# Kernel optimization log

Hardware: AMD Instinct MI355X
Metric: run time of the kernel (lower is better)

The kernel has to match this reference:

```python
import jax, jax.numpy as jnp
import numpy as np

B = 4096
FEATURES = 4608 + 4608 + 8 + 1  # 9225
LSTM = 512
R = FEATURES / LSTM
D1 = int(FEATURES / R ** (1.0 / 3.0))
D2 = int(FEATURES / R ** (2.0 / 3.0))
ACTION_SHAPES = (64, 64, 64, 64, 64, 64, 64, 64)


def setup_inputs() -> dict:
    key = jax.random.key(0)
    ks = jax.random.split(key, 32)
    s = 0.02
    inp = {
        "actualCanvasFeatures": jax.random.normal(ks[0], (B, 4608), jnp.float32),
        "objectiveCanvasFeatures": jax.random.normal(ks[1], (B, 4608), jnp.float32),
        "last_action": jax.random.uniform(ks[2], (B, 8), jnp.float32),
        "episode_percentage": 0,
        # encoder MLP
        "W1": jax.random.normal(ks[3], (FEATURES, D1), jnp.float32) * s,
        "b1": jnp.zeros((D1,), jnp.float32),
        "W2": jax.random.normal(ks[4], (D1, D2), jnp.float32) * s,
        "b2": jnp.zeros((D2,), jnp.float32),
        "W3": jax.random.normal(ks[5], (D2, LSTM), jnp.float32) * s,
        "b3": jnp.zeros((LSTM,), jnp.float32),
        # LSTM (torch gate order i,f,g,o)
        "Wih": jax.random.normal(ks[6], (4 * LSTM, LSTM), jnp.float32) * s,
        "Whh": jax.random.normal(ks[7], (4 * LSTM, LSTM), jnp.float32) * s,
        "bih": jnp.zeros((4 * LSTM,), jnp.float32),
        "bhh": jnp.zeros((4 * LSTM,), jnp.float32),
        "h0": jnp.zeros((B, LSTM), jnp.float32),
        "c0": jnp.zeros((B, LSTM), jnp.float32),
        # decoder
        "dW1": jax.random.normal(ks[8], (LSTM, LSTM // 2), jnp.float32) * s,
        "db1": jnp.zeros((LSTM // 2,), jnp.float32),
        "headWs": tuple(jax.random.normal(ks[9 + i], (LSTM // 2, a), jnp.float32) * s
                        for i, a in enumerate(ACTION_SHAPES)),
        "headbs": tuple(jnp.zeros((a,), jnp.float32) for a in ACTION_SHAPES),
        "dWo": jax.random.normal(ks[20], (LSTM + 1, LSTM), jnp.float32) * s,
        "dbo": jnp.zeros((LSTM,), jnp.float32),
    }
    return inp


def reference(actualCanvasFeatures, objectiveCanvasFeatures, last_action,
              episode_percentage, W1, b1, W2, b2, W3, b3, Wih, Whh, bih, bhh,
              h0, c0, dW1, db1, headWs, headbs, dWo, dbo):
    b = actualCanvasFeatures.shape[0]
    ep = jnp.full((b, 1), episode_percentage, dtype=jnp.float32)
    feats = jnp.concatenate(
        [actualCanvasFeatures, objectiveCanvasFeatures, last_action, ep], axis=1)
    # encoder MLP (dropout is eval-mode identity)
    x = jax.nn.relu(feats @ W1 + b1)
    x = jax.nn.relu(x @ W2 + b2)
    x = jax.nn.relu(x @ W3 + b3)
    # single-step LSTM cell, torch gate order i,f,g,o
    gates = x @ Wih.T + bih + h0 @ Whh.T + bhh
    i, f, g, o = jnp.split(gates, 4, axis=1)
    c = jax.nn.sigmoid(f) * c0 + jax.nn.sigmoid(i) * jnp.tanh(g)
    z = jax.nn.sigmoid(o) * jnp.tanh(c)  # seed
    key = jax.random.key(42)
    actions = []
    log_probabilities = jnp.zeros((b,), jnp.float32)
    entropy = jnp.float32(0.0)
    for Wk, bk in zip(headWs, headbs):
        z1 = jax.nn.relu(z @ dW1 + db1)
        logits = z1 @ Wk + bk
        logp = jax.nn.log_softmax(logits, axis=1)
        probs = jnp.exp(logp)
        key, sk = jax.random.split(key)
        act = jax.random.categorical(sk, logits, axis=1)  # [b] int
        actions.append(act.astype(jnp.float32))
        entropy = entropy + jnp.sum(-jnp.sum(probs * logp, axis=1))
        log_probabilities = log_probabilities + jnp.take_along_axis(
            logp, act[:, None], axis=1)[:, 0]
        z = jax.nn.relu(
            jnp.concatenate([z, act.astype(jnp.float32)[:, None]], axis=1) @ dWo + dbo)
    action = jnp.stack(actions, axis=1)  # [b, n_sub_actions]
    return action, entropy, log_probabilities
```

## Files before the change

kernel.cpp:

```cpp
#include <hip/hip_runtime.h>
#include <cstdint>
#include <cstring>

typedef _Float16 f16;
typedef _Float16 f16x8 __attribute__((ext_vector_type(8)));
typedef float f32x4 __attribute__((ext_vector_type(4)));

static constexpr int kPartitionable = 1;

struct Ptr8 { const float* p[8]; };
struct Keys8 { uint32_t k[8][2]; };

__device__ __host__ __forceinline__ int swz(int r, int k) {
  return k ^ ((r & 7) << 3);
}

__device__ __forceinline__ void gload16(const void* g, void* l) {
  __builtin_amdgcn_global_load_lds(
      (const __attribute__((address_space(1))) unsigned int*)g,
      (__attribute__((address_space(3))) unsigned int*)l, 16, 0, 0);
}

__host__ __device__ inline void tf2x32(uint32_t k0, uint32_t k1,
                                       uint32_t x0, uint32_t x1,
                                       uint32_t& o0, uint32_t& o1) {
  uint32_t ks[3] = {k0, k1, k0 ^ k1 ^ 0x1BD11BDAu};
  uint32_t v0 = x0 + ks[0], v1 = x1 + ks[1];
  const int r0[4] = {13, 15, 26, 6};
  const int r1[4] = {17, 29, 16, 24};
  for (int g = 0; g < 5; ++g) {
    const int* rr = (g & 1) ? r1 : r0;
    for (int j = 0; j < 4; ++j) {
      v0 += v1;
      v1 = (v1 << rr[j]) | (v1 >> (32 - rr[j]));
      v1 ^= v0;
    }
    v0 += ks[(g + 1) % 3];
    v1 += ks[(g + 2) % 3] + (uint32_t)(g + 1);
  }
  o0 = v0; o1 = v1;
}

template <int BM, int BN>
__global__ __launch_bounds__(256, 2) void gemm_split(
    const f16* __restrict__ Ah, const f16* __restrict__ Al, int lda,
    const f16* __restrict__ Bh, const f16* __restrict__ Bl, int ldb,
    int K,
    const float* __restrict__ bias1, const float* __restrict__ bias2,
    int nReal, int relu, int writeF32,
    float* __restrict__ outF, f16* __restrict__ outH, f16* __restrict__ outL,
    int ldo) {
  constexpr int BK = 64;
  constexpr int TM = BM / 32;
  constexpr int TN = BN / 32;
  static_assert(BM == BN, "square tiles only");
  __shared__ f16 sAh[BM * BK];
  __shared__ f16 sAl[BM * BK];
  __shared__ f16 sBh[BN * BK];
  __shared__ f16 sBl[BN * BK];

  const int tid = threadIdx.x;
  const int wave = tid >> 6;
  const int lane = tid & 63;
  const int wm = wave & 1, wn = wave >> 1;
  const int m0 = blockIdx.x * BM;
  const int n0 = blockIdx.y * BN;

  f32x4 acc[TM][TN];
  const f32x4 zero = {0.f, 0.f, 0.f, 0.f};
#pragma unroll
  for (int i = 0; i < TM; ++i)
#pragma unroll
    for (int j = 0; j < TN; ++j) acc[i][j] = zero;

  const f16* src;
  f16* dst;
  int ld, base;
  if (wave == 0)      { src = Ah; dst = sAh; ld = lda; base = m0; }
  else if (wave == 1) { src = Al; dst = sAl; ld = lda; base = m0; }
  else if (wave == 2) { src = Bh; dst = sBh; ld = ldb; base = n0; }
  else                { src = Bl; dst = sBl; ld = ldb; base = n0; }
  constexpr int NITER = BM / 8;
  const f16* gbase = src + (size_t)(base + (lane >> 3)) * ld + (lane & 7) * 8;

  const int fr = lane & 15;
  const int q8 = (lane >> 4) * 8;
  const int sw = (fr & 7) << 3;

  for (int k0 = 0; k0 < K; k0 += BK) {
    __syncthreads();
#pragma unroll
    for (int j = 0; j < NITER; ++j)
      gload16(gbase + (size_t)(j * 8) * ld + k0, dst + j * 512);
    __syncthreads();
#pragma unroll
    for (int kk = 0; kk < BK; kk += 32) {
      const int kf = (kk + q8) ^ sw;
      f16x8 aH[TM], aL[TM], bH[TN], bL[TN];
#pragma unroll
      for (int i = 0; i < TM; ++i) {
        int off = (wm * (BM / 2) + i * 16 + fr) * BK + kf;
        aH[i] = *(const f16x8*)&sAh[off];
        aL[i] = *(const f16x8*)&sAl[off];
      }
#pragma unroll
      for (int j = 0; j < TN; ++j) {
        int off = (wn * (BN / 2) + j * 16 + fr) * BK + kf;
        bH[j] = *(const f16x8*)&sBh[off];
        bL[j] = *(const f16x8*)&sBl[off];
      }
#pragma unroll
      for (int i = 0; i < TM; ++i)
#pragma unroll
        for (int j = 0; j < TN; ++j) {
          acc[i][j] = __builtin_amdgcn_mfma_f32_16x16x32_f16(aH[i], bH[j], acc[i][j], 0, 0, 0);
          acc[i][j] = __builtin_amdgcn_mfma_f32_16x16x32_f16(aH[i], bL[j], acc[i][j], 0, 0, 0);
          acc[i][j] = __builtin_amdgcn_mfma_f32_16x16x32_f16(aL[i], bH[j], acc[i][j], 0, 0, 0);
        }
    }
  }
  const int rq = lane >> 4, cl = lane & 15;
#pragma unroll
  for (int i = 0; i < TM; ++i)
#pragma unroll
    for (int j = 0; j < TN; ++j)
#pragma unroll
      for (int r = 0; r < 4; ++r) {
        int row = m0 + wm * (BM / 2) + i * 16 + rq * 4 + r;
        int col = n0 + wn * (BN / 2) + j * 16 + cl;
        float v = acc[i][j][r];
        if (col < nReal) {
          if (bias1) v += bias1[col];
          if (bias2) v += bias2[col];
          if (relu) v = fmaxf(v, 0.f);
        } else {
          v = 0.f;
        }
        if (writeF32) {
          outF[(size_t)row * ldo + col] = v;
        } else {
          size_t o = (size_t)row * ldo + swz(row, col);
          f16 h = (f16)v;
          outH[o] = h;
          outL[o] = (f16)(v - (float)h);
        }
      }
}

__global__ void conv_feats(const float* __restrict__ A, const float* __restrict__ O,
                           const float* __restrict__ LA, const int* __restrict__ EP,
                           f16* __restrict__ H, f16* __restrict__ L) {
  uint32_t idx = blockIdx.x * 256u + threadIdx.x;
  if (idx >= 4096u * 1160u) return;
  uint32_t b = idx / 1160u;
  uint32_t c = (idx - b * 1160u) * 8u;
  float v[8];
  if (c < 4608u) {
    const float4* p = (const float4*)(A + (size_t)b * 4608 + c);
    float4 x = p[0], y = p[1];
    v[0] = x.x; v[1] = x.y; v[2] = x.z; v[3] = x.w;
    v[4] = y.x; v[5] = y.y; v[6] = y.z; v[7] = y.w;
  } else if (c < 9216u) {
    const float4* p = (const float4*)(O + (size_t)b * 4608 + (c - 4608u));
    float4 x = p[0], y = p[1];
    v[0] = x.x; v[1] = x.y; v[2] = x.z; v[3] = x.w;
    v[4] = y.x; v[5] = y.y; v[6] = y.z; v[7] = y.w;
  } else if (c == 9216u) {
#pragma unroll
    for (int j = 0; j < 8; ++j) v[j] = LA[(size_t)b * 8 + j];
  } else if (c == 9224u) {
    v[0] = (float)EP[0];
#pragma unroll
    for (int j = 1; j < 8; ++j) v[j] = 0.f;
  } else {
#pragma unroll
    for (int j = 0; j < 8; ++j) v[j] = 0.f;
  }
  size_t o = (size_t)b * 9280 + ((int)c ^ (((int)b & 7) << 3));
  f16x8 hv, lv;
#pragma unroll
  for (int j = 0; j < 8; ++j) {
    f16 h = (f16)v[j];
    hv[j] = h;
    lv[j] = (f16)(v[j] - (float)h);
  }
  *(f16x8*)&H[o] = hv;
  *(f16x8*)&L[o] = lv;
}

__global__ void convT_kernel(const float* __restrict__ W, int Kreal, int Nreal,
                             f16* __restrict__ BtH, f16* __restrict__ BtL, int Kpad) {
  __shared__ float tile[32][33];
  int k0 = blockIdx.x * 32, n0 = blockIdx.y * 32;
  int tx = threadIdx.x, ty = threadIdx.y;
  for (int r = 0; r < 32; r += 8) {
    int k = k0 + ty + r, n = n0 + tx;
    float v = (k < Kreal && n < Nreal) ? W[(size_t)k * Nreal + n] : 0.f;
    tile[ty + r][tx] = v;
  }
  __syncthreads();
  for (int r = 0; r < 32; r += 8) {
    int n = n0 + ty + r, k = k0 + tx;
    float v = tile[tx][ty + r];
    size_t o = (size_t)n * Kpad + swz(n, k);
    f16 h = (f16)v;
    BtH[o] = h;
    BtL[o] = (f16)(v - (float)h);
  }
}

__global__ void conv_fm(const float* __restrict__ W, int Kreal, int Nreal, int NT, int KC,
                        f16* __restrict__ FH, f16* __restrict__ FL) {
  int idx = blockIdx.x * 256 + threadIdx.x;
  if (idx >= NT * KC * 64) return;
  int lane = idx & 63;
  int t = idx >> 6;
  int kc = t % KC, ntile = t / KC;
  int n = ntile * 16 + (lane & 15);
  int k0 = kc * 32 + (lane >> 4) * 8;
  f16x8 hv, lv;
#pragma unroll
  for (int j = 0; j < 8; ++j) {
    int k = k0 + j;
    float v = (k < Kreal && n < Nreal) ? W[(size_t)k * Nreal + n] : 0.f;
    f16 h = (f16)v;
    hv[j] = h;
    lv[j] = (f16)(v - (float)h);
  }
  *(f16x8*)&FH[(size_t)idx * 8] = hv;
  *(f16x8*)&FL[(size_t)idx * 8] = lv;
}

__global__ void conv_fm_heads(Ptr8 ws, f16* __restrict__ FH, f16* __restrict__ FL) {
  int h = blockIdx.y;
  int idx = blockIdx.x * 256 + threadIdx.x;
  if (idx >= 2048) return;
  int lane = idx & 63;
  int t = idx >> 6;
  int kc = t & 7, ntile = t >> 3;
  int n = ntile * 16 + (lane & 15);
  int k0 = kc * 32 + (lane >> 4) * 8;
  const float* W = ws.p[h];
  f16x8 hv, lv;
#pragma unroll
  for (int j = 0; j < 8; ++j) {
    float v = W[(size_t)(k0 + j) * 64 + n];
    f16 hh = (f16)v;
    hv[j] = hh;
    lv[j] = (f16)(v - (float)hh);
  }
  size_t base = (size_t)h * 16384 + (size_t)idx * 8;
  *(f16x8*)&FH[base] = hv;
  *(f16x8*)&FL[base] = lv;
}

__global__ void conv_lstmB(const float* __restrict__ Wih, const float* __restrict__ Whh,
                           f16* __restrict__ H, f16* __restrict__ L) {
  uint32_t idx = blockIdx.x * 256u + threadIdx.x;
  uint32_t n = idx >> 10, k = idx & 1023u;
  float v = (k < 512u) ? Wih[(size_t)n * 512 + k] : Whh[(size_t)n * 512 + (k - 512u)];
  size_t o = (size_t)n * 1024 + swz((int)n, (int)k);
  f16 h = (f16)v;
  H[o] = h;
  L[o] = (f16)(v - (float)h);
}

__global__ void conv_h0(const float* __restrict__ h0, f16* __restrict__ H, f16* __restrict__ L) {
  uint32_t idx = blockIdx.x * 256u + threadIdx.x;
  uint32_t b = idx >> 9, j = idx & 511u;
  float v = h0[idx];
  size_t o = (size_t)b * 1024 + swz((int)b, (int)(512 + j));
  f16 h = (f16)v;
  H[o] = h;
  L[o] = (f16)(v - (float)h);
}

__global__ void lstm_pointwise(const float* __restrict__ gates, const float* __restrict__ c0,
                               f16* __restrict__ zH, f16* __restrict__ zL) {
  uint32_t idx = blockIdx.x * 256u + threadIdx.x;
  uint32_t b = idx >> 9, n = idx & 511u;
  const float* g = gates + (size_t)b * 2048;
  float gi = g[n], gf = g[512 + n], gg = g[1024 + n], go = g[1536 + n];
  float si = 1.f / (1.f + expf(-gi));
  float sf = 1.f / (1.f + expf(-gf));
  float so = 1.f / (1.f + expf(-go));
  float c = sf * c0[idx] + si * tanhf(gg);
  float z = so * tanhf(c);
  size_t o = (size_t)b * 576 + swz((int)b, (int)n);
  f16 h = (f16)z;
  zH[o] = h;
  zL[o] = (f16)(z - (float)h);
}

__global__ void init_pads(f16* __restrict__ zAH, f16* __restrict__ zAL,
                          float* __restrict__ out) {
  uint32_t idx = blockIdx.x * 256u + threadIdx.x;
  if (idx < 4096u * 8u) {
    uint32_t b = idx >> 3, c8 = 512u + (idx & 7u) * 8u;
    f16x8 zz = {0, 0, 0, 0, 0, 0, 0, 0};
    *(f16x8*)&zAH[(size_t)b * 576 + c8] = zz;
    *(f16x8*)&zAL[(size_t)b * 576 + c8] = zz;
  }
  if (idx == 0) out[32768] = 0.f;
}

__device__ inline double shfl_xor_dbl(double v, int m) {
  union { double d; int i[2]; } u;
  u.d = v;
  u.i[0] = __shfl_xor(u.i[0], m);
  u.i[1] = __shfl_xor(u.i[1], m);
  return u.d;
}

__global__ __launch_bounds__(256, 1) void decoder_fused(
    const f16* __restrict__ zH0, const f16* __restrict__ zL0,
    const f16* __restrict__ FM1h, const f16* __restrict__ FM1l,
    const float* __restrict__ db1,
    const f16* __restrict__ FMhh, const f16* __restrict__ FMhl,
    Ptr8 hb,
    const f16* __restrict__ FMoh, const f16* __restrict__ FMol,
    const float* __restrict__ dbo,
    Keys8 sk, int partitionable, float* __restrict__ out) {
  constexpr int ZS = 576, Z1S = 256;
  __shared__ f16 zbH[32 * ZS], zbL[32 * ZS];
  __shared__ f16 z1H[32 * Z1S], z1L[32 * Z1S];
  __shared__ float lgt[32 * 64];
  __shared__ float entSh[4];
  const int tid = threadIdx.x;
  const int wave = tid >> 6, lane = tid & 63;
  const int fr = lane & 15, rq = lane >> 4, q8 = rq * 8;
  const int sw = (fr & 7) << 3;
  const int b0 = blockIdx.x * 32;
  const f32x4 zero = {0.f, 0.f, 0.f, 0.f};

  for (int t = tid; t < 2304; t += 256) {
    ((f16x8*)zbH)[t] = ((const f16x8*)(zH0 + (size_t)b0 * ZS))[t];
    ((f16x8*)zbL)[t] = ((const f16x8*)(zL0 + (size_t)b0 * ZS))[t];
  }
  float entAcc = 0.f;
  float logpAcc[8] = {0.f, 0.f, 0.f, 0.f, 0.f, 0.f, 0.f, 0.f};

  for (int h = 0; h < 8; ++h) {
    __syncthreads();
    {
      f32x4 acc[2][4];
#pragma unroll
      for (int i = 0; i < 2; ++i)
#pragma unroll
        for (int j = 0; j < 4; ++j) acc[i][j] = zero;
      for (int kc = 0; kc < 16; ++kc) {
        int kf = (kc * 32 + q8) ^ sw;
        f16x8 aH[2], aL[2];
#pragma unroll
        for (int i = 0; i < 2; ++i) {
          int off = (i * 16 + fr) * ZS + kf;
          aH[i] = *(const f16x8*)&zbH[off];
          aL[i] = *(const f16x8*)&zbL[off];
        }
#pragma unroll
        for (int j = 0; j < 4; ++j) {
          size_t fo = (size_t)((wave * 4 + j) * 16 + kc) * 512 + lane * 8;
          f16x8 bH = *(const f16x8*)&FM1h[fo];
          f16x8 bL = *(const f16x8*)&FM1l[fo];
#pragma unroll
          for (int i = 0; i < 2; ++i) {
            acc[i][j] = __builtin_amdgcn_mfma_f32_16x16x32_f16(aH[i], bH, acc[i][j], 0, 0, 0);
            acc[i][j] = __builtin_amdgcn_mfma_f32_16x16x32_f16(aH[i], bL, acc[i][j], 0, 0, 0);
            acc[i][j] = __builtin_amdgcn_mfma_f32_16x16x32_f16(aL[i], bH, acc[i][j], 0, 0, 0);
          }
        }
      }
#pragma unroll
      for (int j = 0; j < 4; ++j) {
        int col = (wave * 4 + j) * 16 + fr;
        float bb = db1[col];
#pragma unroll
        for (int i = 0; i < 2; ++i)
#pragma unroll
          for (int r = 0; r < 4; ++r) {
            int row = i * 16 + rq * 4 + r;
            float v = fmaxf(acc[i][j][r] + bb, 0.f);
            f16 hv = (f16)v;
            int po = row * Z1S + (col ^ ((row & 7) << 3));
            z1H[po] = hv;
            z1L[po] = (f16)(v - (float)hv);
          }
      }
    }
    __syncthreads();
    {
      f32x4 acc2[2] = {zero, zero};
      const int r0 = (wave & 1) * 16;
      const int tb = (wave >> 1) * 2;
      for (int kc = 0; kc < 8; ++kc) {
        int kf = (kc * 32 + q8) ^ sw;
        int off = (r0 + fr) * Z1S + kf;
        f16x8 aH = *(const f16x8*)&z1H[off];
        f16x8 aL = *(const f16x8*)&z1L[off];
#pragma unroll
        for (int j = 0; j < 2; ++j) {
          size_t fo = (size_t)(h * 32 + (tb + j) * 8 + kc) * 512 + lane * 8;
          f16x8 bH = *(const f16x8*)&FMhh[fo];
          f16x8 bL = *(const f16x8*)&FMhl[fo];
          acc2[j] = __builtin_amdgcn_mfma_f32_16x16x32_f16(aH, bH, acc2[j], 0, 0, 0);
          acc2[j] = __builtin_amdgcn_mfma_f32_16x16x32_f16(aH, bL, acc2[j], 0, 0, 0);
          acc2[j] = __builtin_amdgcn_mfma_f32_16x16x32_f16(aL, bH, acc2[j], 0, 0, 0);
        }
      }
#pragma unroll
      for (int j = 0; j < 2; ++j) {
        int col = (tb + j) * 16 + fr;
        float bb = hb.p[h][col];
#pragma unroll
        for (int r = 0; r < 4; ++r) lgt[(r0 + rq * 4 + r) * 64 + col] = acc2[j][r] + bb;
      }
    }
    __syncthreads();
    for (int rr = 0; rr < 8; ++rr) {
      int row = wave * 8 + rr;
      int b = b0 + row;
      float l = lgt[row * 64 + lane];
      uint32_t i = (uint32_t)b * 64u + (uint32_t)lane;
      uint32_t bits;
      if (partitionable) {
        uint32_t o0, o1;
        tf2x32(sk.k[h][0], sk.k[h][1], 0u, i, o0, o1);
        bits = o0 ^ o1;
      } else {
        const uint32_t Hh = 131072u;
        uint32_t c0, c1, o0, o1;
        int pick;
        if (i < Hh) { c0 = i; c1 = i + Hh; pick = 0; }
        else        { c0 = i - Hh; c1 = i; pick = 1; }
        tf2x32(sk.k[h][0], sk.k[h][1], c0, c1, o0, o1);
        bits = pick ? o1 : o0;
      }
      uint32_t ub = (bits >> 9) | 0x3f800000u;
      float u;
      __builtin_memcpy(&u, &ub, 4);
      u -= 1.0f;
      if (u == 0.0f) u = 1.17549435e-38f;
      double gum = -log(-log((double)u));
      double s = (double)l + gum;
      int bi = lane;
      double bv = s;
#pragma unroll
      for (int off = 1; off < 64; off <<= 1) {
        double ov = shfl_xor_dbl(bv, off);
        int oi = __shfl_xor(bi, off);
        if (ov > bv || (ov == bv && oi < bi)) { bv = ov; bi = oi; }
      }
      int act = bi;
      float m = l;
#pragma unroll
      for (int off = 1; off < 64; off <<= 1) m = fmaxf(m, __shfl_xor(m, off));
      float e = expf(l - m);
      float S = e, D = e * l;
#pragma unroll
      for (int off = 1; off < 64; off <<= 1) {
        S += __shfl_xor(S, off);
        D += __shfl_xor(D, off);
      }
      float M = m + logf(S);
      entAcc += (M - D / S);
      float l_act = __shfl(l, act);
      logpAcc[rr] += (l_act - M);
      if (lane == 0) {
        out[(size_t)b * 8 + h] = (float)act;
        int po = row * ZS + (512 ^ ((row & 7) << 3));
        zbH[po] = (f16)act;
        zbL[po] = (f16)0.f;
      }
    }
    __syncthreads();
    {
      f32x4 acc4[2][8];
#pragma unroll
      for (int i = 0; i < 2; ++i)
#pragma unroll
        for (int j = 0; j < 8; ++j) acc4[i][j] = zero;
      for (int kc = 0; kc < 18; ++kc) {
        int kf = (kc * 32 + q8) ^ sw;
        f16x8 aH[2], aL[2];
#pragma unroll
        for (int i = 0; i < 2; ++i) {
          int off = (i * 16 + fr) * ZS + kf;
          aH[i] = *(const f16x8*)&zbH[off];
          aL[i] = *(const f16x8*)&zbL[off];
        }
#pragma unroll
        for (int j = 0; j < 8; ++j) {
          size_t fo = (size_t)((wave * 8 + j) * 18 + kc) * 512 + lane * 8;
          f16x8 bH = *(const f16x8*)&FMoh[fo];
          f16x8 bL = *(const f16x8*)&FMol[fo];
#pragma unroll
          for (int i = 0; i < 2; ++i) {
            acc4[i][j] = __builtin_amdgcn_mfma_f32_16x16x32_f16(aH[i], bH, acc4[i][j], 0, 0, 0);
            acc4[i][j] = __builtin_amdgcn_mfma_f32_16x16x32_f16(aH[i], bL, acc4[i][j], 0, 0, 0);
            acc4[i][j] = __builtin_amdgcn_mfma_f32_16x16x32_f16(aL[i], bH, acc4[i][j], 0, 0, 0);
          }
        }
      }
      __syncthreads();
#pragma unroll
      for (int j = 0; j < 8; ++j) {
        int col = wave * 128 + j * 16 + fr;
        float bb = dbo[col];
#pragma unroll
        for (int i = 0; i < 2; ++i)
#pragma unroll
          for (int r = 0; r < 4; ++r) {
            int row = i * 16 + rq * 4 + r;
            float v = fmaxf(acc4[i][j][r] + bb, 0.f);
            f16 hv = (f16)v;
            int po = row * ZS + (col ^ ((row & 7) << 3));
            zbH[po] = hv;
            zbL[po] = (f16)(v - (float)hv);
          }
      }
    }
  }
  if (lane == 0) entSh[wave] = entAcc;
  __syncthreads();
  if (tid == 0) atomicAdd(&out[32768], entSh[0] + entSh[1] + entSh[2] + entSh[3]);
  if (lane == 0) {
#pragma unroll
    for (int rr = 0; rr < 8; ++rr) out[32769 + b0 + wave * 8 + rr] = logpAcc[rr];
  }
}

extern "C" void kernel_launch(void* const* d_in, const int* in_sizes, int n_in,
                              void* d_out, int out_size, void* d_ws, size_t ws_size,
                              hipStream_t stream) {
  (void)in_sizes; (void)out_size; (void)ws_size;
  const float* actual = (const float*)d_in[0];
  const float* object = (const float*)d_in[1];
  const float* lastA = (const float*)d_in[2];
  const int* ep = (const int*)d_in[3];
  const float* W1 = (const float*)d_in[4];
  const float* b1 = (const float*)d_in[5];
  const float* W2 = (const float*)d_in[6];
  const float* b2 = (const float*)d_in[7];
  const float* W3 = (const float*)d_in[8];
  const float* b3 = (const float*)d_in[9];
  const float* Wih = (const float*)d_in[10];
  const float* Whh = (const float*)d_in[11];
  const float* bih = (const float*)d_in[12];
  const float* bhh = (const float*)d_in[13];
  const float* h0 = (const float*)d_in[14];
  const float* c0 = (const float*)d_in[15];
  const float* dW1 = (const float*)d_in[16];
  const float* db1 = (const float*)d_in[17];
  const float* headW[8];
  const float* headb[8];
  const float *dWo, *dbo;
  if (n_in >= 36) {
    for (int h = 0; h < 8; ++h) headW[h] = (const float*)d_in[18 + h];
    for (int h = 0; h < 8; ++h) headb[h] = (const float*)d_in[26 + h];
    dWo = (const float*)d_in[34];
    dbo = (const float*)d_in[35];
  } else {
    const float* hw = (const float*)d_in[18];
    const float* hbp = (const float*)d_in[19];
    for (int h = 0; h < 8; ++h) { headW[h] = hw + (size_t)h * 256 * 64; headb[h] = hbp + (size_t)h * 64; }
    dWo = (const float*)d_in[20];
    dbo = (const float*)d_in[21];
  }

  constexpr int Bq = 4096;
  constexpr int K1 = 9280, N1 = 3584, N1r = 3518;
  constexpr int K2 = 3584, N2 = 1408, N2r = 1342;
  constexpr int K3 = 1408, N3 = 512;
  constexpr int KL = 1024, NL = 2048;

  uint8_t* w = (uint8_t*)d_ws;
  size_t off = 0;
  auto alloc = [&](size_t bytes) -> void* {
    off = (off + 1023) & ~(size_t)1023;
    void* p = w + off;
    off += bytes;
    return p;
  };
  f16* A1h = (f16*)alloc((size_t)Bq * K1 * 2);
  f16* A1l = (f16*)alloc((size_t)Bq * K1 * 2);
  f16* Bt1h = (f16*)alloc((size_t)N1 * K1 * 2);
  f16* Bt1l = (f16*)alloc((size_t)N1 * K1 * 2);
  f16* x1h = (f16*)alloc((size_t)Bq * K2 * 2);
  f16* x1l = (f16*)alloc((size_t)Bq * K2 * 2);
  f16* Bt2h = (f16*)alloc((size_t)N2 * K2 * 2);
  f16* Bt2l = (f16*)alloc((size_t)N2 * K2 * 2);
  size_t poff = 0;
  auto palloc = [&](size_t bytes) -> void* {
    poff = (poff + 1023) & ~(size_t)1023;
    void* p = w + poff;
    poff += bytes;
    return p;
  };
  f16* x2h = (f16*)palloc((size_t)Bq * K3 * 2);
  f16* x2l = (f16*)palloc((size_t)Bq * K3 * 2);
  f16* Bt3h = (f16*)palloc((size_t)N3 * K3 * 2);
  f16* Bt3l = (f16*)palloc((size_t)N3 * K3 * 2);
  f16* ALh = (f16*)palloc((size_t)Bq * KL * 2);
  f16* ALl = (f16*)palloc((size_t)Bq * KL * 2);
  f16* BLh = (f16*)palloc((size_t)NL * KL * 2);
  f16* BLl = (f16*)palloc((size_t)NL * KL * 2);
  float* gates = (float*)palloc((size_t)Bq * NL * 4);
  f16* zAH = (f16*)palloc((size_t)Bq * 576 * 2);
  f16* zAL = (f16*)palloc((size_t)Bq * 576 * 2);
  f16* FM1h = (f16*)palloc((size_t)16 * 16 * 512 * 2);
  f16* FM1l = (f16*)palloc((size_t)16 * 16 * 512 * 2);
  f16* FMhh = (f16*)palloc((size_t)8 * 32 * 512 * 2);
  f16* FMhl = (f16*)palloc((size_t)8 * 32 * 512 * 2);
  f16* FMoh = (f16*)palloc((size_t)32 * 18 * 512 * 2);
  f16* FMol = (f16*)palloc((size_t)32 * 18 * 512 * 2);

  uint32_t k0 = 0u, k1 = 42u;
  Keys8 sk;
  for (int h = 0; h < 8; ++h) {
    if (kPartitionable) {
      uint32_t a0, a1, b0v, b1v;
      tf2x32(k0, k1, 0u, 0u, a0, a1);
      tf2x32(k0, k1, 0u, 1u, b0v, b1v);
      sk.k[h][0] = b0v; sk.k[h][1] = b1v;
      k0 = a0; k1 = a1;
    } else {
      uint32_t a0, a1, b0v, b1v;
      tf2x32(k0, k1, 0u, 2u, a0, a1);
      tf2x32(k0, k1, 1u, 3u, b0v, b1v);
      sk.k[h][0] = a1; sk.k[h][1] = b1v;
      k0 = a0; k1 = b0v;
    }
  }
  Ptr8 hws, hbs;
  for (int h = 0; h < 8; ++h) { hws.p[h] = headW[h]; hbs.p[h] = headb[h]; }

  dim3 blk(256);
  dim3 tblk(32, 8);

  conv_feats<<<(4096u * 1160u + 255) / 256, blk, 0, stream>>>(actual, object, lastA, ep, A1h, A1l);
  convT_kernel<<<dim3(K1 / 32, N1 / 32), tblk, 0, stream>>>(W1, 9225, 3518, Bt1h, Bt1l, K1);
  convT_kernel<<<dim3(K2 / 32, N2 / 32), tblk, 0, stream>>>(W2, 3518, 1342, Bt2h, Bt2l, K2);

  gemm_split<128, 128><<<dim3(Bq / 128, N1 / 128), blk, 0, stream>>>(
      A1h, A1l, K1, Bt1h, Bt1l, K1, K1, b1, nullptr, N1r, 1, 0, nullptr, x1h, x1l, K2);

  init_pads<<<(4096u * 8u + 255) / 256, blk, 0, stream>>>(zAH, zAL, (float*)d_out);
  convT_kernel<<<dim3(K3 / 32, N3 / 32), tblk, 0, stream>>>(W3, 1342, 512, Bt3h, Bt3l, K3);
  conv_lstmB<<<(2048u * 1024u) / 256, blk, 0, stream>>>(Wih, Whh, BLh, BLl);
  conv_h0<<<(4096u * 512u) / 256, blk, 0, stream>>>(h0, ALh, ALl);
  conv_fm<<<(16 * 16 * 64 + 255) / 256, blk, 0, stream>>>(dW1, 512, 256, 16, 16, FM1h, FM1l);
  conv_fm<<<(32 * 18 * 64 + 255) / 256, blk, 0, stream>>>(dWo, 513, 512, 32, 18, FMoh, FMol);
  conv_fm_heads<<<dim3(8, 8), blk, 0, stream>>>(hws, FMhh, FMhl);

  gemm_split<128, 128><<<dim3(Bq / 128, N2 / 128), blk, 0, stream>>>(
      x1h, x1l, K2, Bt2h, Bt2l, K2, K2, b2, nullptr, N2r, 1, 0, nullptr, x2h, x2l, K3);
  gemm_split<128, 128><<<dim3(Bq / 128, N3 / 128), blk, 0, stream>>>(
      x2h, x2l, K3, Bt3h, Bt3l, K3, K3, b3, nullptr, N3, 1, 0, nullptr, ALh, ALl, KL);
  gemm_split<128, 128><<<dim3(Bq / 128, NL / 128), blk, 0, stream>>>(
      ALh, ALl, KL, BLh, BLl, KL, KL, bih, bhh, NL, 0, 1, gates, nullptr, nullptr, NL);
  lstm_pointwise<<<(4096u * 512u) / 256, blk, 0, stream>>>(gates, c0, zAH, zAL);

  decoder_fused<<<128, blk, 0, stream>>>(
      zAH, zAL, FM1h, FM1l, db1, FMhh, FMhl, hbs, FMoh, FMol, dbo,
      sk, kPartitionable, (float*)d_out);
}
```

Before: 1.883 ms.

## Double-buffer split GEMM with 8 waves and halve decoder batch per block

The split-fp16 GEMM moves to 512-thread blocks with double-buffered LDS stages, so global-to-LDS loads for the next K tile are issued while the current tile is computed. This replaces the two-barrier load-then-compute loop. Each wave now holds a 64x32 sub-tile, and LDS use grows to 128KB per block, limiting occupancy to one block per CU. Separately, the fused decoder processes 16 rows per block instead of 32 and launches 256 blocks, spreading the serial decode across more CUs at the cost of less weight reuse per block.

```diff
diff --git a/kernel.cpp b/kernel.cpp
--- a/kernel.cpp
+++ b/kernel.cpp
@@ -41,8 +41,7 @@
   o0 = v0; o1 = v1;
 }
 
-template <int BM, int BN>
-__global__ __launch_bounds__(256, 2) void gemm_split(
+__global__ __launch_bounds__(512, 1) void gemm_split(
     const f16* __restrict__ Ah, const f16* __restrict__ Al, int lda,
     const f16* __restrict__ Bh, const f16* __restrict__ Bl, int ldb,
     int K,
@@ -50,84 +49,95 @@
     int nReal, int relu, int writeF32,
     float* __restrict__ outF, f16* __restrict__ outH, f16* __restrict__ outL,
     int ldo) {
-  constexpr int BK = 64;
-  constexpr int TM = BM / 32;
-  constexpr int TN = BN / 32;
-  static_assert(BM == BN, "square tiles only");
-  __shared__ f16 sAh[BM * BK];
-  __shared__ f16 sAl[BM * BK];
-  __shared__ f16 sBh[BN * BK];
-  __shared__ f16 sBl[BN * BK];
+  __shared__ f16 sAh0[8192], sAl0[8192], sBh0[8192], sBl0[8192];
+  __shared__ f16 sAh1[8192], sAl1[8192], sBh1[8192], sBl1[8192];
 
   const int tid = threadIdx.x;
   const int wave = tid >> 6;
   const int lane = tid & 63;
   const int wm = wave & 1, wn = wave >> 1;
-  const int m0 = blockIdx.x * BM;
-  const int n0 = blockIdx.y * BN;
-
-  f32x4 acc[TM][TN];
+  const int m0 = blockIdx.x * 128;
+  const int n0 = blockIdx.y * 128;
+
+  f32x4 acc[4][2];
   const f32x4 zero = {0.f, 0.f, 0.f, 0.f};
 #pragma unroll
-  for (int i = 0; i < TM; ++i)
-#pragma unroll
-    for (int j = 0; j < TN; ++j) acc[i][j] = zero;
-
+  for (int i = 0; i < 4; ++i)
+#pragma unroll
+    for (int j = 0; j < 2; ++j) acc[i][j] = zero;
+
+  const int arr = wave >> 1, p = wave & 1;
   const f16* src;
-  f16* dst;
+  f16 *l0, *l1;
   int ld, base;
-  if (wave == 0)      { src = Ah; dst = sAh; ld = lda; base = m0; }
-  else if (wave == 1) { src = Al; dst = sAl; ld = lda; base = m0; }
-  else if (wave == 2) { src = Bh; dst = sBh; ld = ldb; base = n0; }
-  else                { src = Bl; dst = sBl; ld = ldb; base = n0; }
-  constexpr int NITER = BM / 8;
-  const f16* gbase = src + (size_t)(base + (lane >> 3)) * ld + (lane & 7) * 8;
+  if (arr == 0)      { src = Ah; l0 = sAh0; l1 = sAh1; ld = lda; base = m0; }
+  else if (arr == 1) { src = Al; l0 = sAl0; l1 = sAl1; ld = lda; base = m0; }
+  else if (arr == 2) { src = Bh; l0 = sBh0; l1 = sBh1; ld = ldb; base = n0; }
+  else               { src = Bl; l0 = sBl0; l1 = sBl1; ld = ldb; base = n0; }
+  l0 += p * 4096;
+  l1 += p * 4096;
+  const f16* gbase = src + (size_t)(base + p * 64 + (lane >> 3)) * ld + (lane & 7) * 8;
 
   const int fr = lane & 15;
   const int q8 = (lane >> 4) * 8;
   const int sw = (fr & 7) << 3;
 
-  for (int k0 = 0; k0 < K; k0 += BK) {
-    __syncthreads();
-#pragma unroll
-    for (int j = 0; j < NITER; ++j)
-      gload16(gbase + (size_t)(j * 8) * ld + k0, dst + j * 512);
-    __syncthreads();
-#pragma unroll
-    for (int kk = 0; kk < BK; kk += 32) {
+  auto stage = [&](int k0, f16* lb) {
+#pragma unroll
+    for (int j = 0; j < 8; ++j)
+      gload16(gbase + (size_t)(j * 8) * ld + k0, lb + j * 512);
+  };
+  auto compute = [&](const f16* cAh, const f16* cAl, const f16* cBh, const f16* cBl) {
+#pragma unroll
+    for (int kk = 0; kk < 64; kk += 32) {
       const int kf = (kk + q8) ^ sw;
-      f16x8 aH[TM], aL[TM], bH[TN], bL[TN];
-#pragma unroll
-      for (int i = 0; i < TM; ++i) {
-        int off = (wm * (BM / 2) + i * 16 + fr) * BK + kf;
-        aH[i] = *(const f16x8*)&sAh[off];
-        aL[i] = *(const f16x8*)&sAl[off];
-      }
-#pragma unroll
-      for (int j = 0; j < TN; ++j) {
-        int off = (wn * (BN / 2) + j * 16 + fr) * BK + kf;
-        bH[j] = *(const f16x8*)&sBh[off];
-        bL[j] = *(const f16x8*)&sBl[off];
-      }
-#pragma unroll
-      for (int i = 0; i < TM; ++i)
-#pragma unroll
-        for (int j = 0; j < TN; ++j) {
+      f16x8 aH[4], aL[4], bH[2], bL[2];
+#pragma unroll
+      for (int i = 0; i < 4; ++i) {
+        int off = (wm * 64 + i * 16 + fr) * 64 + kf;
+        aH[i] = *(const f16x8*)&cAh[off];
+        aL[i] = *(const f16x8*)&cAl[off];
+      }
+#pragma unroll
+      for (int j = 0; j < 2; ++j) {
+        int off = (wn * 32 + j * 16 + fr) * 64 + kf;
+        bH[j] = *(const f16x8*)&cBh[off];
+        bL[j] = *(const f16x8*)&cBl[off];
+      }
+#pragma unroll
+      for (int i = 0; i < 4; ++i)
+#pragma unroll
+        for (int j = 0; j < 2; ++j) {
           acc[i][j] = __builtin_amdgcn_mfma_f32_16x16x32_f16(aH[i], bH[j], acc[i][j], 0, 0, 0);
           acc[i][j] = __builtin_amdgcn_mfma_f32_16x16x32_f16(aH[i], bL[j], acc[i][j], 0, 0, 0);
           acc[i][j] = __builtin_amdgcn_mfma_f32_16x16x32_f16(aL[i], bH[j], acc[i][j], 0, 0, 0);
         }
     }
-  }
+  };
+
+  const int nT = K >> 6;
+  stage(0, l0);
+  int t = 0;
+  while (true) {
+    __syncthreads();
+    if (t + 1 < nT) stage((t + 1) * 64, l1);
+    compute(sAh0, sAl0, sBh0, sBl0);
+    if (++t == nT) break;
+    __syncthreads();
+    if (t + 1 < nT) stage((t + 1) * 64, l0);
+    compute(sAh1, sAl1, sBh1, sBl1);
+    if (++t == nT) break;
+  }
+
   const int rq = lane >> 4, cl = lane & 15;
 #pragma unroll
-  for (int i = 0; i < TM; ++i)
-#pragma unroll
-    for (int j = 0; j < TN; ++j)
+  for (int i = 0; i < 4; ++i)
+#pragma unroll
+    for (int j = 0; j < 2; ++j)
 #pragma unroll
       for (int r = 0; r < 4; ++r) {
-        int row = m0 + wm * (BM / 2) + i * 16 + rq * 4 + r;
-        int col = n0 + wn * (BN / 2) + j * 16 + cl;
+        int row = m0 + wm * 64 + i * 16 + rq * 4 + r;
+        int col = n0 + wn * 32 + j * 16 + cl;
         float v = acc[i][j][r];
         if (col < nReal) {
           if (bias1) v += bias1[col];
@@ -322,52 +332,42 @@
     const float* __restrict__ dbo,
     Keys8 sk, int partitionable, float* __restrict__ out) {
   constexpr int ZS = 576, Z1S = 256;
-  __shared__ f16 zbH[32 * ZS], zbL[32 * ZS];
-  __shared__ f16 z1H[32 * Z1S], z1L[32 * Z1S];
-  __shared__ float lgt[32 * 64];
+  __shared__ f16 zbH[16 * ZS], zbL[16 * ZS];
+  __shared__ f16 z1H[16 * Z1S], z1L[16 * Z1S];
+  __shared__ float lgt[16 * 64];
   __shared__ float entSh[4];
   const int tid = threadIdx.x;
   const int wave = tid >> 6, lane = tid & 63;
   const int fr = lane & 15, rq = lane >> 4, q8 = rq * 8;
   const int sw = (fr & 7) << 3;
-  const int b0 = blockIdx.x * 32;
+  const int b0 = blockIdx.x * 16;
   const f32x4 zero = {0.f, 0.f, 0.f, 0.f};
 
-  for (int t = tid; t < 2304; t += 256) {
+  for (int t = tid; t < 1152; t += 256) {
     ((f16x8*)zbH)[t] = ((const f16x8*)(zH0 + (size_t)b0 * ZS))[t];
     ((f16x8*)zbL)[t] = ((const f16x8*)(zL0 + (size_t)b0 * ZS))[t];
   }
   float entAcc = 0.f;
-  float logpAcc[8] = {0.f, 0.f, 0.f, 0.f, 0.f, 0.f, 0.f, 0.f};
+  float logpAcc[4] = {0.f, 0.f, 0.f, 0.f};
 
   for (int h = 0; h < 8; ++h) {
     __syncthreads();
     {
-      f32x4 acc[2][4];
-#pragma unroll
-      for (int i = 0; i < 2; ++i)
-#pragma unroll
-        for (int j = 0; j < 4; ++j) acc[i][j] = zero;
+      f32x4 acc[4];
+#pragma unroll
+      for (int j = 0; j < 4; ++j) acc[j] = zero;
       for (int kc = 0; kc < 16; ++kc) {
         int kf = (kc * 32 + q8) ^ sw;
-        f16x8 aH[2], aL[2];
-#pragma unroll
-        for (int i = 0; i < 2; ++i) {
-          int off = (i * 16 + fr) * ZS + kf;
-          aH[i] = *(const f16x8*)&zbH[off];
-          aL[i] = *(const f16x8*)&zbL[off];
-        }
+        f16x8 aH = *(const f16x8*)&zbH[fr * ZS + kf];
+        f16x8 aL = *(const f16x8*)&zbL[fr * ZS + kf];
 #pragma unroll
         for (int j = 0; j < 4; ++j) {
           size_t fo = (size_t)((wave * 4 + j) * 16 + kc) * 512 + lane * 8;
           f16x8 bH = *(const f16x8*)&FM1h[fo];
           f16x8 bL = *(const f16x8*)&FM1l[fo];
-#pragma unroll
-          for (int i = 0; i < 2; ++i) {
-            acc[i][j] = __builtin_amdgcn_mfma_f32_16x16x32_f16(aH[i], bH, acc[i][j], 0, 0, 0);
-            acc[i][j] = __builtin_amdgcn_mfma_f32_16x16x32_f16(aH[i], bL, acc[i][j], 0, 0, 0);
-            acc[i][j] = __builtin_amdgcn_mfma_f32_16x16x32_f16(aL[i], bH, acc[i][j], 0, 0, 0);
-          }
+          acc[j] = __builtin_amdgcn_mfma_f32_16x16x32_f16(aH, bH, acc[j], 0, 0, 0);
+          acc[j] = __builtin_amdgcn_mfma_f32_16x16x32_f16(aH, bL, acc[j], 0, 0, 0);
+          acc[j] = __builtin_amdgcn_mfma_f32_16x16x32_f16(aL, bH, acc[j], 0, 0, 0);
         }
       }
 #pragma unroll
@@ -375,49 +375,38 @@
         int col = (wave * 4 + j) * 16 + fr;
         float bb = db1[col];
 #pragma unroll
-        for (int i = 0; i < 2; ++i)
-#pragma unroll
-          for (int r = 0; r < 4; ++r) {
-            int row = i * 16 + rq * 4 + r;
-            float v = fmaxf(acc[i][j][r] + bb, 0.f);
-            f16 hv = (f16)v;
-            int po = row * Z1S + (col ^ ((row & 7) << 3));
-            z1H[po] = hv;
-            z1L[po] = (f16)(v - (float)hv);
-          }
+        for (int r = 0; r < 4; ++r) {
+          int row = rq * 4 + r;
+          float v = fmaxf(acc[j][r] + bb, 0.f);
+          f16 hv = (f16)v;
+          int po = row * Z1S + (col ^ ((row & 7) << 3));
+          z1H[po] = hv;
+          z1L[po] = (f16)(v - (float)hv);
+        }
       }
     }
     __syncthreads();
     {
-      f32x4 acc2[2] = {zero, zero};
-      const int r0 = (wave & 1) * 16;
-      const int tb = (wave >> 1) * 2;
+      f32x4 acc2 = zero;
       for (int kc = 0; kc < 8; ++kc) {
         int kf = (kc * 32 + q8) ^ sw;
-        int off = (r0 + fr) * Z1S + kf;
-        f16x8 aH = *(const f16x8*)&z1H[off];
-        f16x8 aL = *(const f16x8*)&z1L[off];
-#pragma unroll
-        for (int j = 0; j < 2; ++j) {
-          size_t fo = (size_t)(h * 32 + (tb + j) * 8 + kc) * 512 + lane * 8;
-          f16x8 bH = *(const f16x8*)&FMhh[fo];
-          f16x8 bL = *(const f16x8*)&FMhl[fo];
-          acc2[j] = __builtin_amdgcn_mfma_f32_16x16x32_f16(aH, bH, acc2[j], 0, 0, 0);
-          acc2[j] = __builtin_amdgcn_mfma_f32_16x16x32_f16(aH, bL, acc2[j], 0, 0, 0);
-          acc2[j] = __builtin_amdgcn_mfma_f32_16x16x32_f16(aL, bH, acc2[j], 0, 0, 0);
-        }
-      }
-#pragma unroll
-      for (int j = 0; j < 2; ++j) {
-        int col = (tb + j) * 16 + fr;
-        float bb = hb.p[h][col];
-#pragma unroll
-        for (int r = 0; r < 4; ++r) lgt[(r0 + rq * 4 + r) * 64 + col] = acc2[j][r] + bb;
-      }
+        f16x8 aH = *(const f16x8*)&z1H[fr * Z1S + kf];
+        f16x8 aL = *(const f16x8*)&z1L[fr * Z1S + kf];
+        size_t fo = (size_t)(h * 32 + wave * 8 + kc) * 512 + lane * 8;
+        f16x8 bH = *(const f16x8*)&FMhh[fo];
+        f16x8 bL = *(const f16x8*)&FMhl[fo];
+        acc2 = __builtin_amdgcn_mfma_f32_16x16x32_f16(aH, bH, acc2, 0, 0, 0);
+        acc2 = __builtin_amdgcn_mfma_f32_16x16x32_f16(aH, bL, acc2, 0, 0, 0);
+        acc2 = __builtin_amdgcn_mfma_f32_16x16x32_f16(aL, bH, acc2, 0, 0, 0);
+      }
+      int col = wave * 16 + fr;
+      float bb = hb.p[h][col];
+#pragma unroll
+      for (int r = 0; r < 4; ++r) lgt[(rq * 4 + r) * 64 + col] = acc2[r] + bb;
     }
     __syncthreads();
-    for (int rr = 0; rr < 8; ++rr) {
-      int row = wave * 8 + rr;
+    for (int rr = 0; rr < 4; ++rr) {
+      int row = wave * 4 + rr;
       int b = b0 + row;
       float l = lgt[row * 64 + lane];
       uint32_t i = (uint32_t)b * 64u + (uint32_t)lane;
@@ -474,31 +463,21 @@
     }
     __syncthreads();
     {
-      f32x4 acc4[2][8];
-#pragma unroll
-      for (int i = 0; i < 2; ++i)
-#pragma unroll
-        for (int j = 0; j < 8; ++j) acc4[i][j] = zero;
+      f32x4 acc4[8];
+#pragma unroll
+      for (int j = 0; j < 8; ++j) acc4[j] = zero;
       for (int kc = 0; kc < 18; ++kc) {
         int kf = (kc * 32 + q8) ^ sw;
-        f16x8 aH[2], aL[2];
-#pragma unroll
-        for (int i = 0; i < 2; ++i) {
-          int off = (i * 16 + fr) * ZS + kf;
-          aH[i] = *(const f16x8*)&zbH[off];
-          aL[i] = *(const f16x8*)&zbL[off];
-        }
+        f16x8 aH = *(const f16x8*)&zbH[fr * ZS + kf];
+        f16x8 aL = *(const f16x8*)&zbL[fr * ZS + kf];
 #pragma unroll
         for (int j = 0; j < 8; ++j) {
           size_t fo = (size_t)((wave * 8 + j) * 18 + kc) * 512 + lane * 8;
           f16x8 bH = *(const f16x8*)&FMoh[fo];
           f16x8 bL = *(const f16x8*)&FMol[fo];
-#pragma unroll
-          for (int i = 0; i < 2; ++i) {
-            acc4[i][j] = __builtin_amdgcn_mfma_f32_16x16x32_f16(aH[i], bH, acc4[i][j], 0, 0, 0);
-            acc4[i][j] = __builtin_amdgcn_mfma_f32_16x16x32_f16(aH[i], bL, acc4[i][j], 0, 0, 0);
-            acc4[i][j] = __builtin_amdgcn_mfma_f32_16x16x32_f16(aL[i], bH, acc4[i][j], 0, 0, 0);
-          }
+          acc4[j] = __builtin_amdgcn_mfma_f32_16x16x32_f16(aH, bH, acc4[j], 0, 0, 0);
+          acc4[j] = __builtin_amdgcn_mfma_f32_16x16x32_f16(aH, bL, acc4[j], 0, 0, 0);
+          acc4[j] = __builtin_amdgcn_mfma_f32_16x16x32_f16(aL, bH, acc4[j], 0, 0, 0);
         }
       }
       __syncthreads();
@@ -507,16 +486,14 @@
         int col = wave * 128 + j * 16 + fr;
         float bb = dbo[col];
 #pragma unroll
-        for (int i = 0; i < 2; ++i)
-#pragma unroll
-          for (int r = 0; r < 4; ++r) {
-            int row = i * 16 + rq * 4 + r;
-            float v = fmaxf(acc4[i][j][r] + bb, 0.f);
-            f16 hv = (f16)v;
-            int po = row * ZS + (col ^ ((row & 7) << 3));
-            zbH[po] = hv;
-            zbL[po] = (f16)(v - (float)hv);
-          }
+        for (int r = 0; r < 4; ++r) {
+          int row = rq * 4 + r;
+          float v = fmaxf(acc4[j][r] + bb, 0.f);
+          f16 hv = (f16)v;
+          int po = row * ZS + (col ^ ((row & 7) << 3));
+          zbH[po] = hv;
+          zbL[po] = (f16)(v - (float)hv);
+        }
       }
     }
   }
@@ -525,7 +502,7 @@
   if (tid == 0) atomicAdd(&out[32768], entSh[0] + entSh[1] + entSh[2] + entSh[3]);
   if (lane == 0) {
 #pragma unroll
-    for (int rr = 0; rr < 8; ++rr) out[32769 + b0 + wave * 8 + rr] = logpAcc[rr];
+    for (int rr = 0; rr < 4; ++rr) out[32769 + b0 + wave * 4 + rr] = logpAcc[rr];
   }
 }
 
@@ -635,13 +612,14 @@
   for (int h = 0; h < 8; ++h) { hws.p[h] = headW[h]; hbs.p[h] = headb[h]; }
 
   dim3 blk(256);
+  dim3 blkG(512);
   dim3 tblk(32, 8);
 
   conv_feats<<<(4096u * 1160u + 255) / 256, blk, 0, stream>>>(actual, object, lastA, ep, A1h, A1l);
   convT_kernel<<<dim3(K1 / 32, N1 / 32), tblk, 0, stream>>>(W1, 9225, 3518, Bt1h, Bt1l, K1);
   convT_kernel<<<dim3(K2 / 32, N2 / 32), tblk, 0, stream>>>(W2, 3518, 1342, Bt2h, Bt2l, K2);
 
-  gemm_split<128, 128><<<dim3(Bq / 128, N1 / 128), blk, 0, stream>>>(
+  gemm_split<<<dim3(Bq / 128, N1 / 128), blkG, 0, stream>>>(
       A1h, A1l, K1, Bt1h, Bt1l, K1, K1, b1, nullptr, N1r, 1, 0, nullptr, x1h, x1l, K2);
 
   init_pads<<<(4096u * 8u + 255) / 256, blk, 0, stream>>>(zAH, zAL, (float*)d_out);
@@ -652,15 +630,15 @@
   conv_fm<<<(32 * 18 * 64 + 255) / 256, blk, 0, stream>>>(dWo, 513, 512, 32, 18, FMoh, FMol);
   conv_fm_heads<<<dim3(8, 8), blk, 0, stream>>>(hws, FMhh, FMhl);
 
-  gemm_split<128, 128><<<dim3(Bq / 128, N2 / 128), blk, 0, stream>>>(
+  gemm_split<<<dim3(Bq / 128, N2 / 128), blkG, 0, stream>>>(
       x1h, x1l, K2, Bt2h, Bt2l, K2, K2, b2, nullptr, N2r, 1, 0, nullptr, x2h, x2l, K3);
-  gemm_split<128, 128><<<dim3(Bq / 128, N3 / 128), blk, 0, stream>>>(
+  gemm_split<<<dim3(Bq / 128, N3 / 128), blkG, 0, stream>>>(
       x2h, x2l, K3, Bt3h, Bt3l, K3, K3, b3, nullptr, N3, 1, 0, nullptr, ALh, ALl, KL);
-  gemm_split<128, 128><<<dim3(Bq / 128, NL / 128), blk, 0, stream>>>(
+  gemm_split<<<dim3(Bq / 128, NL / 128), blkG, 0, stream>>>(
       ALh, ALl, KL, BLh, BLl, KL, KL, bih, bhh, NL, 0, 1, gates, nullptr, nullptr, NL);
   lstm_pointwise<<<(4096u * 512u) / 256, blk, 0, stream>>>(gates, c0, zAH, zAL);
 
-  decoder_fused<<<128, blk, 0, stream>>>(
+  decoder_fused<<<256, blk, 0, stream>>>(
       zAH, zAL, FM1h, FM1l, db1, FMhh, FMhl, hbs, FMoh, FMol, dbo,
       sk, kPartitionable, (float*)d_out);
 }
```

Result: slower. 2.182 ms (+15.9%).
